# Performance work log

Hardware: AMD Instinct MI355X
Metric: run time of the kernel (lower is better)

The kernel has to match this reference:

```python
import jax, jax.numpy as jnp
import numpy as np

N = 4096
DEG = 16.0
KC = 64  # max closed-neighborhood size supported (deg~16 graph => safe)


def setup_inputs() -> dict:
    key = jax.random.key(0)
    ks = jax.random.split(key, 6)
    u = jax.random.uniform(ks[0], (N, N))
    upper = jnp.triu((u < (DEG / N)).astype(jnp.float32), k=1)
    adj = upper + upper.T  # symmetric 0/1, zero diagonal
    d = 64
    return {
        'adj': adj,
        'e_w': jax.random.normal(ks[1], (15, d), dtype=jnp.float32) * 0.25,
        'e_b': jnp.zeros((d,), jnp.float32),
        'w1': jax.random.normal(ks[2], (3, d, d), dtype=jnp.float32) * 0.125,
        'b1': jnp.zeros((3, d), jnp.float32),
        'w2': jax.random.normal(ks[3], (3, d, d), dtype=jnp.float32) * 0.125,
        'b2': jnp.zeros((3, d), jnp.float32),
        'eps': jnp.zeros((3,), jnp.float32),
    }


def cr_feat(adj):
    n = adj.shape[0]
    m = adj + jnp.eye(n, dtype=adj.dtype)  # closed-neighborhood indicator rows [N,N]
    k = m.sum(1)                            # |S_v|
    D = m @ adj                             # D[v,u] = degree of u inside S_v (A symmetric)
    E = 0.5 * jnp.sum(m * D, axis=1)        # edges inside S_v
    W = jnp.sum(m * D * (D - 1.0) * 0.5, axis=1)  # wedges inside S_v
    vals, idx = jax.lax.top_k(m, KC)        # members of S_v (padded)
    valid = (vals > 0.5).astype(adj.dtype)
    sub = adj[idx[:, :, None], idx[:, None, :]]        # [N,KC,KC] induced subgraph
    sub = sub * valid[:, :, None] * valid[:, None, :]
    T = jnp.einsum('vij,vjk,vki->v', sub, sub, sub) / 6.0  # triangles inside S_v
    f3 = T
    f2 = W - 3.0 * T
    f1 = E * (k - 2.0) - 2.0 * f2 - 3.0 * f3
    tot = k * (k - 1.0) * (k - 2.0) / 6.0   # C(k,3) = total triples
    f0 = tot - f1 - f2 - f3
    f = jnp.stack([f0, f1, f2, f3], axis=1)
    f = jnp.where((k >= 3.0)[:, None], f, 0.0)  # original skips |nb|<3
    return f / (jnp.sum(f, axis=1, keepdims=True) + 1e-10)


def ww_feat(adj):
    a2 = adj @ adj
    a4 = a2 @ a2                             # matrix_power(adj, 4)
    vals, _ = jax.lax.top_k(a4, 8)           # per-row sort desc, top 8
    return vals


def degree_feat(adj):
    d = adj.sum(1)
    diag_a2 = jnp.einsum('vu,uv->v', adj, adj)  # diag(A@A)
    return jnp.stack([d, d ** 2, diag_a2], axis=1)


def _forward(adj, e_w, e_b, w1, b1, w2, b2, eps):
    feats = jnp.concatenate([cr_feat(adj), ww_feat(adj), degree_feat(adj)], axis=1)  # [N,15]
    x = feats @ e_w + e_b
    for i in range(3):
        h = (1.0 + eps[i]) * x + adj @ x
        x = jax.nn.relu(h @ w1[i] + b1[i]) @ w2[i] + b2[i]
    return x.sum(0)


def reference(adj, e_w, e_b, w1, b1, w2, b2, eps):
    return _forward(adj, e_w, e_b, w1, b1, w2, b2, eps)
```

## Files before the change

### kernel.cpp

```cpp
#include <hip/hip_runtime.h>
#include <hip/hip_bf16.h>
#include <stdint.h>

#define NN 4096


__device__ __forceinline__ unsigned int wave_umax_bcast(unsigned int v) {
    int x = (int)v;
    x = max(x, __builtin_amdgcn_update_dpp(0, x, 0x111, 0xF, 0xF, true));
    x = max(x, __builtin_amdgcn_update_dpp(0, x, 0x112, 0xF, 0xF, true));
    x = max(x, __builtin_amdgcn_update_dpp(0, x, 0x114, 0xF, 0xF, true));
    x = max(x, __builtin_amdgcn_update_dpp(0, x, 0x118, 0xF, 0xF, true));
    x = max(x, __builtin_amdgcn_update_dpp(0, x, 0x142, 0xF, 0xF, true));
    x = max(x, __builtin_amdgcn_update_dpp(0, x, 0x143, 0xF, 0xF, true));
    return (unsigned int)__builtin_amdgcn_readlane(x, 63);
}

__global__ __launch_bounds__(256) void scan_k(const float* __restrict__ adj,
                                              int* __restrict__ nbr,
                                              int* __restrict__ deg,
                                              unsigned long long* __restrict__ abits,
                                              float* __restrict__ feats) {
    __shared__ int nlist[4][64];
    int tid = threadIdx.x;
    int wv = tid >> 6, ln = tid & 63;
    int v = blockIdx.x * 4 + wv;
    size_t rb = (size_t)v * NN;
    int total = 0;
    unsigned long long w0 = 0;
    const float4* row4 = (const float4*)(adj + rb);
    for (int base = 0; base < NN; base += 256) {
        float4 f = row4[(base >> 2) + ln];
        int q4 = (base >> 8) << 2;
        #pragma unroll
        for (int j = 0; j < 4; j++) {
            float vj = (j == 0) ? f.x : (j == 1) ? f.y : (j == 2) ? f.z : f.w;
            unsigned long long m = __ballot(vj > 0.5f);
            if (vj > 0.5f) {
                int pos = total + __popcll(m & ((1ull << ln) - 1ull));
                if (pos < 64) nlist[wv][pos] = base + 4 * ln + j;
            }
            if (ln == q4 + j) w0 = m;
            total += __popcll(m);
        }
    }
    abits[(size_t)v * 64 + ln] = w0;
    int degL = min(total, 64);
    if (ln < degL) nbr[v * 64 + ln] = nlist[wv][ln];
    if (ln == 0) {
        deg[v] = total;
        float degf = (float)total;
        feats[v * 16 + 12] = degf;
        feats[v * 16 + 13] = degf * degf;
        feats[v * 16 + 14] = degf;
    }
}

__global__ __launch_bounds__(256) void cra2_k(const unsigned long long* __restrict__ abits,
                                              const int* __restrict__ nbr,
                                              const int* __restrict__ deg,
                                              unsigned int* __restrict__ a3n,
                                              unsigned int* __restrict__ side,
                                              unsigned int* __restrict__ scnt,
                                              float* __restrict__ feats) {
    __shared__ __align__(64) unsigned int smem[NN + 132 + 640];
    int tid = threadIdx.x;
    int bid = blockIdx.x;
    int wv = tid >> 6, ln = tid & 63;

    if (bid < NN) {
        unsigned int* acc   = smem;
        int* us             = (int*)(smem + NN);
        int* dus            = (int*)(smem + NN + 64);
        unsigned int* wsumS = smem + NN + 128;
        unsigned int* srcL  = smem + NN + 132;
        int v = bid;
        uint4 z = {0u, 0u, 0u, 0u};
        #pragma unroll
        for (int i = 0; i < 4; i++) ((uint4*)acc)[tid + 256 * i] = z;
        int dv = min(deg[v], 64);
        if (tid < dv) {
            int u = nbr[v * 64 + tid];
            us[tid] = u;
            dus[tid] = min(deg[u], 64);
        }
        __syncthreads();
        for (int p = tid; p < dv * 64; p += 256) {
            int i = p >> 6, wi = p & 63;
            if (wi < dus[i]) atomicAdd(&acc[nbr[us[i] * 64 + wi]], 1u);
        }
        __syncthreads();
        unsigned int myw[16];
        int local = 0;
        #pragma unroll
        for (int m = 0; m < 16; m++) {
            unsigned int a = acc[tid + 256 * m];
            myw[m] = a;
            local += (a != 0u);
        }
        int incl = local;
        #pragma unroll
        for (int off = 1; off < 64; off <<= 1) {
            int n = __shfl_up(incl, off, 64);
            if (ln >= off) incl += n;
        }
        if (ln == 63) wsumS[wv] = (unsigned int)incl;
        __syncthreads();
        unsigned int wpre = 0, nsrc = 0;
        #pragma unroll
        for (int q = 0; q < 4; q++) {
            unsigned int s = wsumS[q];
            if (q < wv) wpre += s;
            nsrc += s;
        }
        unsigned int pos = wpre + (unsigned int)(incl - local);
        #pragma unroll
        for (int m = 0; m < 16; m++) {
            unsigned int a = myw[m];
            if (a) {
                unsigned int col = (unsigned int)tid + 256u * m;
                unsigned int dgu = (unsigned int)min(deg[col], 64);
                if (pos < 640u) srcL[pos] = (a << 19) | (dgu << 12) | col;
                pos++;
            }
        }
        if (nsrc > 640u) nsrc = 640u;
        __syncthreads();
        #pragma unroll
        for (int i = 0; i < 4; i++) ((uint4*)acc)[tid + 256 * i] = z;
        __syncthreads();
        int lim64 = (((int)nsrc + 1) >> 1) << 6;
        for (int q = tid; q < lim64; q += 256) {
            int s = ((q >> 6) << 1) | ((q >> 5) & 1);
            int j = q & 31;
            if (s < (int)nsrc) {
                unsigned int e = srcL[s];
                int dgu = (int)((e >> 12) & 0x7Fu);
                unsigned int w = e >> 19;
                const int* nru = nbr + (e & 0xFFFu) * 64;
                if (j < dgu) atomicAdd(&acc[nru[j]], w);
                if (j == 31) {
                    for (int jj = 32; jj < dgu; jj++) atomicAdd(&acc[nru[jj]], w);
                }
            }
        }
        __syncthreads();
        unsigned int wA = 0, wB = 0, ovm = 0;
        #pragma unroll
        for (int k = 0; k < 8; k++) {
            unsigned int a = acc[tid + 512 * k];
            wA |= min(a, 15u) << (4 * k);
            ovm |= (a > 15u ? 1u : 0u) << k;
        }
        #pragma unroll
        for (int k = 0; k < 8; k++) {
            unsigned int a = acc[tid + 256 + 512 * k];
            wB |= min(a, 15u) << (4 * k);
            ovm |= (a > 15u ? 1u : 0u) << (8 + k);
        }
        a3n[(size_t)v * 512 + tid] = wA;
        a3n[(size_t)v * 512 + tid + 256] = wB;
        int lov = __popc(ovm);
        int inc2 = lov;
        #pragma unroll
        for (int off = 1; off < 64; off <<= 1) {
            int n = __shfl_up(inc2, off, 64);
            if (ln >= off) inc2 += n;
        }
        if (ln == 63) wsumS[wv] = (unsigned int)inc2;
        __syncthreads();
        unsigned int wpre2 = 0, totS = 0;
        #pragma unroll
        for (int q = 0; q < 4; q++) {
            unsigned int s = wsumS[q];
            if (q < wv) wpre2 += s;
            totS += s;
        }
        unsigned int pos2 = wpre2 + (unsigned int)(inc2 - lov);
        unsigned int* sideR = side + (size_t)v * 192;
        while (ovm) {
            int i2 = __ffs(ovm) - 1;
            ovm &= ovm - 1;
            unsigned int col = (i2 < 8) ? (unsigned int)(tid + 512 * i2)
                                        : (unsigned int)(tid + 256 + 512 * (i2 - 8));
            unsigned int a = acc[col];
            if (pos2 < 192u) sideR[pos2] = ((a - 15u) << 16) | col;
            pos2++;
        }
        if (tid == 0) scnt[v] = min(totS, 192u);
    } else {
        unsigned long long* rows = (unsigned long long*)smem;
        int* mems = (int*)(smem + 1024);
        int v = (bid - NN) * 4 + wv;

        int dv = deg[v];
        int degL = min(dv, 64);
        int c = min(dv + 1, 64);

        int nl = (ln < degL) ? nbr[v * 64 + ln] : 0;
        int isless = (ln < degL && nl < v) ? 1 : 0;
        int pos = isless;
        #pragma unroll
        for (int off = 32; off; off >>= 1) pos += __shfl_xor(pos, off, 64);

        int mem = 0;
        if (ln < c) {
            if (ln < pos)       mem = nl;
            else if (ln == pos) mem = v;
            else                mem = nbr[v * 64 + ln - 1];
        }
        mems[wv * 64 + ln] = mem;
        __syncthreads();

        unsigned long long mask = 0ull;
        {
            const unsigned long long* rowb = abits + (size_t)mem * 64;
            for (int j = 0; j < c; j++) {
                int mj = mems[wv * 64 + j];
                unsigned long long w = rowb[((mj >> 8) << 2) | (mj & 3)];
                mask |= ((w >> ((mj >> 2) & 63)) & 1ull) << j;
            }
        }
        if (ln >= c) mask = 0ull;
        rows[wv * 64 + ln] = mask;
        __syncthreads();

        int tpart = 0;
        float epart = 0.f, wpart = 0.f;
        if (ln < c) {
            unsigned long long mm = mask;
            while (mm) {
                int j = __ffsll(mm) - 1;
                mm &= mm - 1;
                tpart += __popcll(mask & rows[wv * 64 + j]);
            }
            if (ln != pos) {
                int cn = __popcll(rows[wv * 64 + pos] & mask);
                float D2 = (float)cn + 1.0f;
                epart = D2;
                wpart = D2 * (D2 - 1.0f) * 0.5f;
            }
        }
        float es = epart, wsum2 = wpart;
        int ts = tpart;
        #pragma unroll
        for (int off = 32; off; off >>= 1) {
            es += __shfl_xor(es, off, 64);
            wsum2 += __shfl_xor(wsum2, off, 64);
            ts += __shfl_xor(ts, off, 64);
        }

        if (ln == 0) {
            float degf = (float)dv;
            float k = degf + 1.0f;
            float E = 0.5f * (es + degf);
            float W = wsum2 + degf * (degf - 1.0f) * 0.5f;
            float T = (float)ts / 6.0f;
            float f3 = T;
            float f2 = W - 3.0f * T;
            float f1 = E * (k - 2.0f) - 2.0f * f2 - 3.0f * f3;
            float tot2 = k * (k - 1.0f) * (k - 2.0f) / 6.0f;
            float f0 = tot2 - f1 - f2 - f3;
            if (k < 3.0f) { f0 = f1 = f2 = f3 = 0.f; }
            float s = f0 + f1 + f2 + f3 + 1e-10f;
            feats[v * 16 + 0] = f0 / s;
            feats[v * 16 + 1] = f1 / s;
            feats[v * 16 + 2] = f2 / s;
            feats[v * 16 + 3] = f3 / s;
        }
    }
}

__global__ __launch_bounds__(512) void a4row_k(const unsigned int* __restrict__ a3n,
                                               const unsigned int* __restrict__ side,
                                               const unsigned int* __restrict__ scnt,
                                               const int* __restrict__ deg,
                                               const int* __restrict__ nbr,
                                               const float* __restrict__ feats,
                                               const float* __restrict__ e_w,
                                               const float* __restrict__ e_b,
                                               float* __restrict__ x0) {
    __shared__ unsigned int sacc[NN];
    __shared__ unsigned int sbase[64];
    __shared__ unsigned int sbs[64];
    __shared__ unsigned int sS[64];
    __shared__ unsigned int wtops[64];
    int tid = threadIdx.x;
    int wv = tid >> 6, ln = tid & 63;
    int v = blockIdx.x;

    {
        uint4 z = {0u, 0u, 0u, 0u};
        ((uint4*)sacc)[tid] = z;
        ((uint4*)sacc)[tid + 512] = z;
    }
    int dvv = min(deg[v], 64);
    if (tid < dvv) {
        unsigned int u = (unsigned int)nbr[v * 64 + tid];
        sbase[tid] = u * 512u;
        sbs[tid]   = u * 192u;
        sS[tid]    = scnt[u];
    }
    __syncthreads();

    for (int i = wv; i < dvv; i += 8) {
        int ns = (int)sS[i];
        const unsigned int* sp = side + sbs[i];
        for (int g2 = ln; g2 < ns; g2 += 64) {
            unsigned int e = sp[g2];
            atomicAdd(&sacc[e & 0xFFFu], e >> 16);
        }
    }

    unsigned int aE = 0, aO = 0;
    unsigned int SE0 = 0, SE1 = 0, SO0 = 0, SO1 = 0;
    for (int s0 = 0; s0 < dvv; s0 += 16) {
        int se = min(s0 + 16, dvv);
        for (int s = s0; s < se; s++) {
            unsigned int w = a3n[sbase[s] + (unsigned int)tid];
            aE += w & 0x0F0F0F0Fu;
            aO += (w >> 4) & 0x0F0F0F0Fu;
        }
        SE0 += __builtin_amdgcn_perm(0u, aE, 0x0c010c00u);
        SE1 += __builtin_amdgcn_perm(0u, aE, 0x0c030c02u);
        SO0 += __builtin_amdgcn_perm(0u, aO, 0x0c010c00u);
        SO1 += __builtin_amdgcn_perm(0u, aO, 0x0c030c02u);
        aE = 0; aO = 0;
    }
    __syncthreads();

    unsigned int vv[8];
    vv[0] = (SE0 & 0xFFFFu) + sacc[tid];
    vv[1] = (SO0 & 0xFFFFu) + sacc[tid + 512];
    vv[2] = (SE0 >> 16)     + sacc[tid + 1024];
    vv[3] = (SO0 >> 16)     + sacc[tid + 1536];
    vv[4] = (SE1 & 0xFFFFu) + sacc[tid + 2048];
    vv[5] = (SO1 & 0xFFFFu) + sacc[tid + 2560];
    vv[6] = (SE1 >> 16)     + sacc[tid + 3072];
    vv[7] = (SO1 >> 16)     + sacc[tid + 3584];

    unsigned int best[8];
    #pragma unroll
    for (int q = 0; q < 8; q++) best[q] = 0u;
    #pragma unroll
    for (int m = 0; m < 8; m++) {
        unsigned int val = vv[m];
        if (val > best[7]) {
            best[7] = val;
            #pragma unroll
            for (int s = 7; s > 0; s--) {
                if (best[s] > best[s - 1]) {
                    unsigned int t2 = best[s - 1]; best[s - 1] = best[s]; best[s] = t2;
                } else break;
            }
        }
    }

    unsigned int wave_val = 0u;
    #pragma unroll
    for (int r = 0; r < 8; r++) {
        unsigned int m = wave_umax_bcast(best[0]);
        unsigned long long bb = __ballot(best[0] == m);
        int src = __ffsll(bb) - 1;
        if (ln == src) {
            #pragma unroll
            for (int s = 0; s < 7; s++) best[s] = best[s + 1];
            best[7] = 0u;
        }
        if (ln == r) wave_val = m;
    }
    if (ln < 8) wtops[wv * 8 + ln] = wave_val;
    __syncthreads();

    if (wv == 0) {
        unsigned int cand = wtops[ln];
        unsigned int myv = 0u;
        #pragma unroll
        for (int r = 0; r < 8; r++) {
            unsigned int m = wave_umax_bcast(cand);
            unsigned long long bb = __ballot(cand == m);
            int src = __ffsll(bb) - 1;
            if (ln == src) cand = 0u;
            if (ln == r) myv = m;
        }
        int d = ln;
        float s = e_b[d];
        s += feats[v * 16 + 0]  * e_w[0 * 64 + d];
        s += feats[v * 16 + 1]  * e_w[1 * 64 + d];
        s += feats[v * 16 + 2]  * e_w[2 * 64 + d];
        s += feats[v * 16 + 3]  * e_w[3 * 64 + d];
        #pragma unroll
        for (int j = 0; j < 8; j++) {
            float mj = (float)(unsigned int)__shfl((int)myv, j, 64);
            s += mj * e_w[(4 + j) * 64 + d];
        }
        s += feats[v * 16 + 12] * e_w[12 * 64 + d];
        s += feats[v * 16 + 13] * e_w[13 * 64 + d];
        s += feats[v * 16 + 14] * e_w[14 * 64 + d];
        x0[(size_t)v * 64 + d] = s;
    }
}

__global__ __launch_bounds__(256) void layer_k(const float* __restrict__ xin,
                                               float* __restrict__ xout,
                                               const float* __restrict__ w1,
                                               const float* __restrict__ b1,
                                               const float* __restrict__ w2,
                                               const float* __restrict__ b2,
                                               const float* __restrict__ eps,
                                               const int* __restrict__ nbr,
                                               const int* __restrict__ deg,
                                               float* __restrict__ out,
                                               int li) {
    __shared__ float wL[4096];
    __shared__ float h[4][64], t[4][64];
    int tid = threadIdx.x;
    int wv = tid >> 6, d = tid & 63;
    int v = blockIdx.x * 4 + wv;

    {
        const float4* src = (const float4*)(w1 + li * 4096);
        #pragma unroll
        for (int i = 0; i < 4; i++) ((float4*)wL)[tid + 256 * i] = src[tid + 256 * i];
    }

    float xv = xin[(size_t)v * 64 + d];
    int dv = min(deg[v], 64);
    const int* nl = nbr + v * 64;
    float agg = 0.f;
    int j = 0;
    for (; j + 4 <= dv; j += 4) {
        int n0 = nl[j], n1 = nl[j + 1], n2 = nl[j + 2], n3 = nl[j + 3];
        float a0 = xin[(size_t)n0 * 64 + d];
        float a1 = xin[(size_t)n1 * 64 + d];
        float a2v = xin[(size_t)n2 * 64 + d];
        float a3 = xin[(size_t)n3 * 64 + d];
        agg += (a0 + a1) + (a2v + a3);
    }
    for (; j < dv; j++) agg += xin[(size_t)nl[j] * 64 + d];
    float hv = (1.0f + eps[li]) * xv + agg;
    h[wv][d] = hv;
    __syncthreads();

    float s = b1[li * 64 + d];
    #pragma unroll 8
    for (int k = 0; k < 64; k++) s += h[wv][k] * wL[k * 64 + d];
    s = fmaxf(s, 0.f);
    t[wv][d] = s;
    __syncthreads();

    {
        const float4* src = (const float4*)(w2 + li * 4096);
        #pragma unroll
        for (int i = 0; i < 4; i++) ((float4*)wL)[tid + 256 * i] = src[tid + 256 * i];
    }
    __syncthreads();

    float o = b2[li * 64 + d];
    #pragma unroll 8
    for (int k = 0; k < 64; k++) o += t[wv][k] * wL[k * 64 + d];
    if (li == 2) {
        h[wv][d] = o;
        __syncthreads();
        if (wv == 0)
            atomicAdd(&out[d], (h[0][d] + h[1][d]) + (h[2][d] + h[3][d]));
    } else {
        xout[(size_t)v * 64 + d] = o;
    }
}

extern "C" void kernel_launch(void* const* d_in, const int* in_sizes, int n_in,
                              void* d_out, int out_size, void* d_ws, size_t ws_size,
                              hipStream_t stream) {
    const float* adj = (const float*)d_in[0];
    const float* e_w = (const float*)d_in[1];
    const float* e_b = (const float*)d_in[2];
    const float* w1  = (const float*)d_in[3];
    const float* b1  = (const float*)d_in[4];
    const float* w2  = (const float*)d_in[5];
    const float* b2  = (const float*)d_in[6];
    const float* eps = (const float*)d_in[7];
    float* out = (float*)d_out;

    char* ws = (char*)d_ws;
    unsigned int*       a3n     = (unsigned int*)(ws);
    unsigned int*       side    = (unsigned int*)(ws + 8388608);
    unsigned int*       scnt    = (unsigned int*)(ws + 11534336);
    int*                nbr     = (int*)(ws + 25165824);
    int*                deg     = (int*)(ws + 26214400);
    float*              feats   = (float*)(ws + 26247168);
    float*              x0      = (float*)(ws + 26509312);
    float*              x1      = (float*)(ws + 27557888);
    unsigned long long* abits   = (unsigned long long*)(ws + 28868608);

    hipMemsetAsync(out, 0, 64 * sizeof(float), stream);
    scan_k<<<1024, 256, 0, stream>>>(adj, nbr, deg, abits, feats);
    cra2_k<<<5120, 256, 0, stream>>>(abits, nbr, deg, a3n, side, scnt, feats);
    a4row_k<<<4096, 512, 0, stream>>>(a3n, side, scnt, deg, nbr, feats, e_w, e_b, x0);
    layer_k<<<1024, 256, 0, stream>>>(x0, x1, w1, b1, w2, b2, eps, nbr, deg, out, 0);
    layer_k<<<1024, 256, 0, stream>>>(x1, x0, w1, b1, w2, b2, eps, nbr, deg, out, 1);
    layer_k<<<1024, 256, 0, stream>>>(x0, x1, w1, b1, w2, b2, eps, nbr, deg, out, 2);
}
```

Measured before the change: 253.2 us.

## Enumerate 2-walk pairs directly instead of dense A² accumulation and compaction

The A³ row computation previously built a dense A² row in shared memory with atomics, scanned it to compact nonzero sources with weights, cleared it, then scattered weighted neighbor lists. It now prefix-sums neighbor degrees to place every (neighbor, neighbor-of-neighbor) pair directly into a list, then scatters unit atomics per pair. This removes one dense atomic pass, a 4096-entry scan, a compaction and two barriers. In exchange, duplicate paths are no longer merged, so more pairs and atomics are issued, and the 640-entry cap now truncates raw pairs rather than distinct sources, which may drop contributions for high-degree neighborhoods.

```diff
diff --git a/kernel.cpp b/kernel.cpp
--- a/kernel.cpp
+++ b/kernel.cpp
@@ -63,7 +63,7 @@
                                               unsigned int* __restrict__ side,
                                               unsigned int* __restrict__ scnt,
                                               float* __restrict__ feats) {
-    __shared__ __align__(64) unsigned int smem[NN + 132 + 640];
+    __shared__ __align__(64) unsigned int smem[NN + 196 + 640];
     int tid = threadIdx.x;
     int bid = blockIdx.x;
     int wv = tid >> 6, ln = tid & 63;
@@ -72,75 +72,52 @@
         unsigned int* acc   = smem;
         int* us             = (int*)(smem + NN);
         int* dus            = (int*)(smem + NN + 64);
-        unsigned int* wsumS = smem + NN + 128;
-        unsigned int* srcL  = smem + NN + 132;
+        unsigned int* pbase = smem + NN + 128;
+        unsigned int* wsumS = smem + NN + 192;
+        unsigned int* plist = smem + NN + 196;
         int v = bid;
         uint4 z = {0u, 0u, 0u, 0u};
         #pragma unroll
         for (int i = 0; i < 4; i++) ((uint4*)acc)[tid + 256 * i] = z;
         int dv = min(deg[v], 64);
-        if (tid < dv) {
-            int u = nbr[v * 64 + tid];
+        if (tid < 64) {
+            int u = (tid < dv) ? nbr[v * 64 + tid] : 0;
             us[tid] = u;
-            dus[tid] = min(deg[u], 64);
-        }
-        __syncthreads();
+            int du = (tid < dv) ? min(deg[u], 64) : 0;
+            dus[tid] = du;
+            int incl = du;
+            #pragma unroll
+            for (int off = 1; off < 64; off <<= 1) {
+                int n = __shfl_up(incl, off, 64);
+                if (tid >= off) incl += n;
+            }
+            pbase[tid] = (unsigned int)(incl - du);
+            if (tid == 63) wsumS[0] = (unsigned int)incl;
+        }
+        __syncthreads();
+        int npair = (int)min(wsumS[0], 640u);
         for (int p = tid; p < dv * 64; p += 256) {
-            int i = p >> 6, wi = p & 63;
-            if (wi < dus[i]) atomicAdd(&acc[nbr[us[i] * 64 + wi]], 1u);
-        }
-        __syncthreads();
-        unsigned int myw[16];
-        int local = 0;
-        #pragma unroll
-        for (int m = 0; m < 16; m++) {
-            unsigned int a = acc[tid + 256 * m];
-            myw[m] = a;
-            local += (a != 0u);
-        }
-        int incl = local;
-        #pragma unroll
-        for (int off = 1; off < 64; off <<= 1) {
-            int n = __shfl_up(incl, off, 64);
-            if (ln >= off) incl += n;
-        }
-        if (ln == 63) wsumS[wv] = (unsigned int)incl;
-        __syncthreads();
-        unsigned int wpre = 0, nsrc = 0;
-        #pragma unroll
-        for (int q = 0; q < 4; q++) {
-            unsigned int s = wsumS[q];
-            if (q < wv) wpre += s;
-            nsrc += s;
-        }
-        unsigned int pos = wpre + (unsigned int)(incl - local);
-        #pragma unroll
-        for (int m = 0; m < 16; m++) {
-            unsigned int a = myw[m];
-            if (a) {
-                unsigned int col = (unsigned int)tid + 256u * m;
-                unsigned int dgu = (unsigned int)min(deg[col], 64);
-                if (pos < 640u) srcL[pos] = (a << 19) | (dgu << 12) | col;
-                pos++;
-            }
-        }
-        if (nsrc > 640u) nsrc = 640u;
-        __syncthreads();
-        #pragma unroll
-        for (int i = 0; i < 4; i++) ((uint4*)acc)[tid + 256 * i] = z;
-        __syncthreads();
-        int lim64 = (((int)nsrc + 1) >> 1) << 6;
+            int i = p >> 6, j = p & 63;
+            if (j < dus[i]) {
+                unsigned int pos = pbase[i] + (unsigned int)j;
+                if (pos < 640u) {
+                    unsigned int w = (unsigned int)nbr[us[i] * 64 + j];
+                    plist[pos] = w | ((unsigned int)min(deg[w], 64) << 12);
+                }
+            }
+        }
+        __syncthreads();
+        int lim64 = ((npair + 1) >> 1) << 6;
         for (int q = tid; q < lim64; q += 256) {
             int s = ((q >> 6) << 1) | ((q >> 5) & 1);
             int j = q & 31;
-            if (s < (int)nsrc) {
-                unsigned int e = srcL[s];
-                int dgu = (int)((e >> 12) & 0x7Fu);
-                unsigned int w = e >> 19;
-                const int* nru = nbr + (e & 0xFFFu) * 64;
-                if (j < dgu) atomicAdd(&acc[nru[j]], w);
+            if (s < npair) {
+                unsigned int e = plist[s];
+                int dgw = (int)(e >> 12);
+                const int* nrw = nbr + (e & 0xFFFu) * 64;
+                if (j < dgw) atomicAdd(&acc[nrw[j]], 1u);
                 if (j == 31) {
-                    for (int jj = 32; jj < dgu; jj++) atomicAdd(&acc[nru[jj]], w);
+                    for (int jj = 32; jj < dgw; jj++) atomicAdd(&acc[nrw[jj]], 1u);
                 }
             }
         }
```

Result: no change. 249.2 us (-1.6%).
